# Optimization experiments

Measured on AMD Instinct MI355X. Metric: run time of the kernel, lower is better.

## Reference

```python
import jax, jax.numpy as jnp
import numpy as np

NGRAM = 2
NUM_HEADS = 16
NUM_BUCKETS = 32
EMBED_DIM = 1024
REAL_T = 512
BSZ = 4


def setup_inputs() -> dict:
    key = jax.random.key(0)
    ks = jax.random.split(key, 10)
    tgt_len = (1 + NGRAM) * REAL_T
    E, H, NB = EMBED_DIM, NUM_HEADS, NUM_BUCKETS
    w = 0.02
    return {
        "query": jax.random.normal(ks[0], (tgt_len, BSZ, E), jnp.float32),
        "self_attn_mask": jnp.zeros((REAL_T, REAL_T), jnp.float32),
        "ngram_mask_matrix": jnp.zeros((NGRAM, REAL_T, 2 * REAL_T), jnp.float32),
        "i_buckets_main_stream": jax.random.randint(ks[1], (BSZ, REAL_T, REAL_T), 0, NB, jnp.int32),
        "i_bucket_relative_stream": jax.random.randint(ks[2], (BSZ, REAL_T, 2 * REAL_T), 0, NB, jnp.int32),
        "in_proj_weight": jax.random.normal(ks[3], (3 * E, E), jnp.float32) * w,
        "in_proj_bias": jnp.zeros((3 * E,), jnp.float32),
        "out_proj_weight": jax.random.normal(ks[4], (E, E), jnp.float32) * w,
        "out_proj_bias": jnp.zeros((E,), jnp.float32),
        "relative_weight": jax.random.normal(ks[5], (NB * H, E), jnp.float32) * w,
        "relative_bias": jnp.zeros((NB * H,), jnp.float32),
    }


def _forward(query, self_attn_mask, ngram_mask_matrix,
             ib_main, ib_rel,
             in_proj_weight, in_proj_bias, out_proj_weight, out_proj_bias,
             relative_weight, relative_bias):
    tgt_len, bsz, E = query.shape
    H, n = NUM_HEADS, NGRAM
    hd = E // H
    nb = relative_weight.shape[0] // H
    T = tgt_len // (1 + n)
    scaling = hd ** -0.5

    # fused qkv projection
    qkv = query @ in_proj_weight.T + in_proj_bias  # [tgt, B, 3E]
    q, k, v = jnp.split(qkv, 3, axis=-1)
    q = q * scaling

    def to_bh(x):  # [tgt, B, E] -> [B*H, tgt, hd]
        return x.reshape(tgt_len, bsz * H, hd).transpose(1, 0, 2)
    q, k, v = to_bh(q), to_bh(k), to_bh(v)

    h_main = query[:T]                                  # [T, B, E]
    h_pred = query[T:].reshape(n, T, bsz, E)            # [n, T, B, E]
    q_main, k_main, v_main = q[:, :T], k[:, :T], v[:, :T]            # [BH, T, hd]
    def pred(x):  # [BH, n*T, hd] -> [n, BH, T, hd]
        return x[:, T:].reshape(bsz * H, n, T, hd).transpose(1, 0, 2, 3)
    q_pred, k_pred, v_pred = pred(q), pred(k), pred(v)

    # ---- main stream ----
    aw_main = jnp.einsum('bth,bsh->bts', q_main, k_main)  # [BH, T, T]
    # relative bias: per-token bucket values gathered by bucket index
    vals_main = h_main.transpose(1, 0, 2) @ relative_weight.T + relative_bias  # [B, T, nb*H]
    vals_main = vals_main.reshape(bsz, T, nb, H).transpose(0, 3, 1, 2)         # [B, H, T, nb]
    ib = jnp.broadcast_to(ib_main[:, None].astype(jnp.int32), (bsz, H, T, T))
    rel_main = jnp.take_along_axis(vals_main, ib, axis=-1).reshape(bsz * H, T, T)
    aw_main = aw_main + rel_main + self_attn_mask[None]
    p_main = jax.nn.softmax(aw_main, axis=-1)
    attn_main = jnp.einsum('bts,bsh->bth', p_main, v_main)  # [BH, T, hd]
    attn_main = attn_main.transpose(1, 0, 2).reshape(T, bsz, E)

    # ---- ngram predict streams ----
    k_ng = jnp.concatenate([jnp.broadcast_to(k_main[None], (n,) + k_main.shape), k_pred], axis=2)  # [n, BH, 2T, hd]
    v_ng = jnp.concatenate([jnp.broadcast_to(v_main[None], (n,) + v_main.shape), v_pred], axis=2)
    aw_ng = jnp.einsum('nbtc,nbsc->nbts', q_pred, k_ng)  # [n, BH, T, 2T]

    vals_ng = h_pred.transpose(0, 2, 1, 3) @ relative_weight.T + relative_bias  # [n, B, T, nb*H]
    vals_ng = vals_ng.reshape(n, bsz, T, nb, H).transpose(0, 1, 4, 2, 3)        # [n, B, H, T, nb]
    ibr = jnp.broadcast_to(ib_rel[None, :, None].astype(jnp.int32), (n, bsz, H, T, 2 * T))
    rel_ng = jnp.take_along_axis(vals_ng, ibr, axis=-1).reshape(n, bsz * H, T, 2 * T)
    aw_ng = aw_ng + rel_ng + ngram_mask_matrix[:, None]
    p_ng = jax.nn.softmax(aw_ng, axis=-1)
    attn_ng = jnp.einsum('nbts,nbsc->nbtc', p_ng, v_ng)  # [n, BH, T, hd]
    attn_ng = attn_ng.transpose(0, 2, 1, 3).reshape(n * T, bsz, E)

    attn = jnp.concatenate([attn_main, attn_ng], axis=0)  # [tgt, B, E]
    return attn @ out_proj_weight.T + out_proj_bias


def reference(query, self_attn_mask, ngram_mask_matrix,
              i_buckets_main_stream, i_bucket_relative_stream,
              in_proj_weight, in_proj_bias, out_proj_weight, out_proj_bias,
              relative_weight, relative_bias):
    return _forward(query, self_attn_mask, ngram_mask_matrix,
                    i_buckets_main_stream, i_bucket_relative_stream,
                    in_proj_weight, in_proj_bias, out_proj_weight, out_proj_bias,
                    relative_weight, relative_bias)
```

## Files before the change

### kernel.cpp

```cpp
#include <hip/hip_runtime.h>

#define TSEQ 512
#define BSZN 4
#define NH 16
#define NBN 32
#define EMB 1024
#define HD 64
#define TGT 1536
#define MROWS 6144
#define LOG2E 1.44269504088896f

typedef unsigned short ushort_t;
typedef __bf16 bf8 __attribute__((ext_vector_type(8)));
typedef __bf16 bf2_t __attribute__((ext_vector_type(2)));
typedef ushort_t u16x8v __attribute__((ext_vector_type(8)));
typedef unsigned int u32x2 __attribute__((ext_vector_type(2)));
typedef float f32x4 __attribute__((ext_vector_type(4)));

__device__ __forceinline__ unsigned short f2bf(float f) {
  return __builtin_bit_cast(unsigned short, (__bf16)f);
}

__device__ __forceinline__ float bf2f(unsigned short u) {
  return __builtin_bit_cast(float, (unsigned int)u << 16);
}

__device__ __forceinline__ unsigned int packbf(float a, float b) {
  bf2_t t;
  t[0] = (__bf16)a;
  t[1] = (__bf16)b;
  return __builtin_bit_cast(unsigned int, t);
}

__device__ __forceinline__ void gload16(const void* g, void* l) {
  __builtin_amdgcn_global_load_lds(
      (const __attribute__((address_space(1))) void*)g,
      (__attribute__((address_space(3))) void*)l, 16, 0, 0);
}

__device__ __forceinline__ f32x4 mfma_bf16(bf8 a, bf8 b, f32x4 c) {
  return __builtin_amdgcn_mfma_f32_16x16x32_bf16(a, b, c, 0, 0, 0);
}

__device__ __forceinline__ float lanebcast(float v, int srclane) {
  return __builtin_bit_cast(float,
      __builtin_amdgcn_ds_bpermute(srclane * 4, __builtin_bit_cast(int, v)));
}

__global__ void prep_all_kernel(const float* __restrict__ q, const float* __restrict__ win,
                                const float* __restrict__ wout, const float* __restrict__ wrel,
                                const int* __restrict__ ibm, const int* __restrict__ ibr,
                                const float* __restrict__ mm, const float* __restrict__ mng,
                                ushort_t* __restrict__ qo, ushort_t* __restrict__ wino,
                                ushort_t* __restrict__ wouto, ushort_t* __restrict__ wrelo,
                                unsigned int* __restrict__ cm, unsigned int* __restrict__ cng) {
  const int i = blockIdx.x * blockDim.x + threadIdx.x;
  const int n0 = 1572864, n1 = 786432, n2 = 262144, n3 = 131072;
  const int ncvt = n0 + n1 + n2 + n3;
  const int nm = 262144, nr = 1048576;
  if (i < ncvt) {
    const float* src;
    ushort_t* dst;
    int off;
    if (i < n0) { src = q; dst = qo; off = i; }
    else if (i < n0 + n1) { src = win; dst = wino; off = i - n0; }
    else if (i < n0 + n1 + n2) { src = wout; dst = wouto; off = i - n0 - n1; }
    else { src = wrel; dst = wrelo; off = i - n0 - n1 - n2; }
    const float4 v = reinterpret_cast<const float4*>(src)[off];
    ushort4 o;
    o.x = f2bf(v.x); o.y = f2bf(v.y); o.z = f2bf(v.z); o.w = f2bf(v.w);
    reinterpret_cast<ushort4*>(dst)[off] = o;
  } else if (i < ncvt + nm) {
    const int f = (i - ncvt) * 4;
    const int4 ib = *reinterpret_cast<const int4*>(ibm + f);
    const float4 mk = *reinterpret_cast<const float4*>(mm + (f & 262143));
    uint4 o;
    o.x = ((unsigned int)f2bf(mk.x * LOG2E) << 16) | ((unsigned int)ib.x & 31u);
    o.y = ((unsigned int)f2bf(mk.y * LOG2E) << 16) | ((unsigned int)ib.y & 31u);
    o.z = ((unsigned int)f2bf(mk.z * LOG2E) << 16) | ((unsigned int)ib.z & 31u);
    o.w = ((unsigned int)f2bf(mk.w * LOG2E) << 16) | ((unsigned int)ib.w & 31u);
    *reinterpret_cast<uint4*>(cm + f) = o;
  } else if (i < ncvt + nm + nr) {
    const int f = (i - ncvt - nm) * 4;
    const int ib_off = ((f >> 20) << 19) + (f & 524287);
    const int mk_off = f & 1048575;
    const int4 ib = *reinterpret_cast<const int4*>(ibr + ib_off);
    const float4 mk = *reinterpret_cast<const float4*>(mng + mk_off);
    uint4 o;
    o.x = ((unsigned int)f2bf(mk.x * LOG2E) << 16) | ((unsigned int)ib.x & 31u);
    o.y = ((unsigned int)f2bf(mk.y * LOG2E) << 16) | ((unsigned int)ib.y & 31u);
    o.z = ((unsigned int)f2bf(mk.z * LOG2E) << 16) | ((unsigned int)ib.z & 31u);
    o.w = ((unsigned int)f2bf(mk.w * LOG2E) << 16) | ((unsigned int)ib.w & 31u);
    *reinterpret_cast<uint4*>(cng + f) = o;
  }
}

template <int MODE>
__global__ __launch_bounds__(256) void gemm_bt(
    const ushort_t* __restrict__ A, const ushort_t* __restrict__ B,
    const float* __restrict__ bias, float* __restrict__ Cf,
    ushort_t* __restrict__ Qo, ushort_t* __restrict__ Ko, ushort_t* __restrict__ Vto,
    int M, int N, int K) {
  __shared__ ushort_t lds[16384];
  ushort_t* lA = lds;
  ushort_t* lB = lds + 8192;

  const int tid = threadIdx.x;
  const int lane = tid & 63;
  const int wid = tid >> 6;
  const int l15 = lane & 15, l4 = lane >> 4;
  const int bm = blockIdx.y, bn = blockIdx.x;
  const int wm = (wid >> 1) * 64, wn = (wid & 1) * 64;

  f32x4 acc[4][4] = {};

  const int r8 = tid >> 3;
  const int c8 = ((tid & 7) ^ (r8 & 7)) * 8;
  const ushort_t* Ag = A + (size_t)(bm * 128 + r8) * K + c8;
  const ushort_t* Bg = B + (size_t)(bn * 128 + r8) * K + c8;
  ushort_t* lAp = lA + tid * 8;
  ushort_t* lBp = lB + tid * 8;

  for (int kt = 0; kt < K; kt += 64) {
    __syncthreads();
#pragma unroll
    for (int i = 0; i < 4; ++i) {
      gload16(Ag + (size_t)i * 32 * K + kt, lAp + i * 2048);
      gload16(Bg + (size_t)i * 32 * K + kt, lBp + i * 2048);
    }
    __syncthreads();
#pragma unroll
    for (int k0 = 0; k0 < 2; ++k0) {
      bf8 af[4], bv[4];
#pragma unroll
      for (int mi = 0; mi < 4; ++mi) {
        const int row = wm + mi * 16 + l15;
        const int slot = (k0 * 4 + l4) ^ (row & 7);
        af[mi] = *reinterpret_cast<const bf8*>(lA + row * 64 + slot * 8);
      }
#pragma unroll
      for (int ni = 0; ni < 4; ++ni) {
        const int row = wn + ni * 16 + l15;
        const int slot = (k0 * 4 + l4) ^ (row & 7);
        bv[ni] = *reinterpret_cast<const bf8*>(lB + row * 64 + slot * 8);
      }
#pragma unroll
      for (int mi = 0; mi < 4; ++mi)
#pragma unroll
        for (int ni = 0; ni < 4; ++ni)
          acc[mi][ni] = mfma_bf16(af[mi], bv[ni], acc[mi][ni]);
    }
  }

  if (MODE == 0 && bn >= 16) {
    __syncthreads();
    char* tb = reinterpret_cast<char*>(lds);
#pragma unroll
    for (int ni = 0; ni < 4; ++ni) {
      const int colloc = wn + ni * 16 + l15;
      const float bc = bias[bn * 128 + colloc];
      const unsigned int swz = (colloc & 7) << 4;
#pragma unroll
      for (int mi = 0; mi < 4; ++mi) {
        const int t_loc = (wm >> 2) + mi * 4 + l4;
        f32x4 v = acc[mi][ni];
#pragma unroll
        for (int r = 0; r < 4; ++r) {
          const int byteoff = colloc * 256 + ((r * 64 + t_loc * 2) ^ swz);
          *reinterpret_cast<ushort_t*>(tb + byteoff) = f2bf(v[r] + bc);
        }
      }
    }
    __syncthreads();
    const int tglob0 = bm * 32;
#pragma unroll
    for (int p = 0; p < 2; ++p) {
      const int pair = wid * 2 + p;
      const int bb = pair >> 1;
      const int hl = pair & 1;
      const int hh = (bn - 16) * 2 + hl;
      const int bh = bb * NH + hh;
      const int tch = lane & 3;
#pragma unroll
      for (int ii = 0; ii < 4; ++ii) {
        const int dloc = ii * 16 + (lane >> 2);
        const int colloc = hl * 64 + dloc;
        const int byteoff = colloc * 256 + ((bb * 64 + tch * 16) ^ ((colloc & 7) << 4));
        const u16x8v val = *reinterpret_cast<const u16x8v*>(tb + byteoff);
        *reinterpret_cast<u16x8v*>(
            Vto + ((size_t)bh * HD + dloc) * TGT + tglob0 + tch * 8) = val;
      }
    }
    return;
  }

#pragma unroll
  for (int ni = 0; ni < 4; ++ni) {
    const int col = bn * 128 + wn + ni * 16 + l15;
    const float bc = bias[col];
#pragma unroll
    for (int mi = 0; mi < 4; ++mi) {
      const int row0 = bm * 128 + wm + mi * 16 + l4 * 4;
      f32x4 v = acc[mi][ni];
#pragma unroll
      for (int r = 0; r < 4; ++r) {
        const int row = row0 + r;
        float val = v[r] + bc;
        if (MODE == 0) {
          const int part = col >> 10;
          const int cc = col & 1023;
          const int h = cc >> 6, d = cc & 63;
          const int t = row >> 2, bb = row & 3;
          const int bh = bb * NH + h;
          if (part == 0) {
            Qo[((size_t)bh * TGT + t) * HD + d] = f2bf(val * (0.125f * LOG2E));
          } else {
            Ko[((size_t)bh * TGT + t) * HD + d] = f2bf(val);
          }
        } else if (MODE == 3) {
          const int hh = col & 15, nb = col >> 4;
          const int qg = row >> 2, bb2 = row & 3;
          Qo[(((size_t)(bb2 * NH + hh)) * TGT + qg) * NBN + nb] = f2bf(val * LOG2E);
        } else {
          Cf[(size_t)row * N + col] = val;
        }
      }
    }
  }
}

__global__ __launch_bounds__(256, 3) void attn_kernel(
    const ushort_t* __restrict__ Q, const ushort_t* __restrict__ Kb,
    const ushort_t* __restrict__ Vt, const ushort_t* __restrict__ VMh,
    const unsigned int* __restrict__ comb_main, const unsigned int* __restrict__ comb_ng,
    ushort_t* __restrict__ AT) {
  __shared__ unsigned char kbuf[2][8192];
  __shared__ unsigned char vbuf[2][8192];
  __shared__ ushort_t vmt[4][1024];
  __shared__ unsigned int pbl[4][512];

  const int tid = threadIdx.x;
  const int lane = tid & 63, wid = tid >> 6;
  const int l15 = lane & 15, l4 = lane >> 4;

  const int n = blockIdx.x;
  const int xcd = n & 7;
  const int b = xcd >> 1;
  const int idx = (xcd & 1) * 96 + (n >> 3);
  const int h = idx / 12;
  const int rem = idx - h * 12;
  const int z = rem >> 2;
  const int blk = rem & 3;
  const int g = (z == 0) ? 0 : z - 1;
  const int bh = b * NH + h;
  const int t0 = blk * 128 + wid * 32;
  const int qrow0 = (z == 0) ? t0 : TSEQ + g * TSEQ + t0;
  const int nsb = (z == 0) ? 8 : 16;

  gload16(VMh + ((size_t)bh * TGT + qrow0 + (lane >> 2)) * NBN + (lane & 3) * 8,
          (ushort_t*)vmt[wid] + lane * 8);
  gload16(VMh + ((size_t)bh * TGT + qrow0 + 16 + (lane >> 2)) * NBN + (lane & 3) * 8,
          (ushort_t*)vmt[wid] + 512 + lane * 8);

  bf8 qf[2][2];
#pragma unroll
  for (int th = 0; th < 2; ++th)
#pragma unroll
    for (int hf = 0; hf < 2; ++hf)
      qf[th][hf] = *reinterpret_cast<const bf8*>(
          &Q[((size_t)bh * TGT + qrow0 + th * 16 + l15) * HD + hf * 32 + l4 * 8]);

  const unsigned int* cb[2];
  {
    const unsigned int* cbase = (z == 0)
        ? comb_main + (size_t)b * TSEQ * TSEQ
        : comb_ng + (size_t)(b * 2 + g) * TSEQ * (2 * TSEQ);
    const int sstr = (z == 0) ? TSEQ : 2 * TSEQ;
    cb[0] = cbase + (size_t)(t0 + l15) * sstr;
    cb[1] = cbase + (size_t)(t0 + 16 + l15) * sstr;
  }

  float m_run[2] = {-1e30f, -1e30f};
  float l_run[2] = {0.f, 0.f};
  f32x4 oacc[2][4] = {};

  const int r8 = lane >> 3;
  const int swzs = ((lane & 7) ^ r8) << 4;
  const int swzr = (l15 & 7) << 4;
  const int swz2 = (l15 & 7) << 2;

  auto stage = [&](int sb, int bf) {
    const int srow0 = (sb < 8) ? sb * 64 : TSEQ + g * TSEQ + (sb - 8) * 64;
    const ushort_t* ks = Kb + ((size_t)bh * TGT + srow0 + wid * 16 + r8) * HD + (swzs >> 1);
    gload16(ks, &kbuf[bf][wid * 2048 + lane * 16]);
    gload16(ks + 8 * HD, &kbuf[bf][wid * 2048 + 1024 + lane * 16]);
    const ushort_t* vs = Vt + ((size_t)bh * HD + wid * 16 + r8) * TGT + srow0 + (swzs >> 1);
    gload16(vs, &vbuf[bf][wid * 2048 + lane * 16]);
    gload16(vs + 8 * TGT, &vbuf[bf][wid * 2048 + 1024 + lane * 16]);
  };

  stage(0, 0);
  asm volatile("s_waitcnt vmcnt(0)" ::: "memory");
  __builtin_amdgcn_s_barrier();

  int cur = 0;
  for (int sb = 0; sb < nsb; ++sb) {
    const int scol = sb * 64;
    if (sb + 1 < nsb) stage(sb + 1, cur ^ 1);

    const unsigned char* kb = kbuf[cur];
    const unsigned char* vbb = vbuf[cur];

    bf8 kf[4][2];
#pragma unroll
    for (int j = 0; j < 4; ++j) {
      const int row = j * 16 + l15;
      kf[j][0] = *reinterpret_cast<const bf8*>(kb + row * 128 + ((l4 * 16) ^ swzr));
      kf[j][1] = *reinterpret_cast<const bf8*>(kb + row * 128 + ((64 + l4 * 16) ^ swzr));
    }

#pragma unroll
    for (int th = 0; th < 2; ++th) {
      const unsigned int* cwp = cb[th] + scol + l4 * 4;
      const uint4 c0 = *reinterpret_cast<const uint4*>(cwp);
      const uint4 c1 = *reinterpret_cast<const uint4*>(cwp + 16);
      const uint4 c2 = *reinterpret_cast<const uint4*>(cwp + 32);
      const uint4 c3 = *reinterpret_cast<const uint4*>(cwp + 48);
      const unsigned int cwa[4][4] = {{c0.x, c0.y, c0.z, c0.w},
                                      {c1.x, c1.y, c1.z, c1.w},
                                      {c2.x, c2.y, c2.z, c2.w},
                                      {c3.x, c3.y, c3.z, c3.w}};
      f32x4 st[4];
#pragma unroll
      for (int j = 0; j < 4; ++j) {
        f32x4 s4 = {};
        s4 = mfma_bf16(kf[j][0], qf[th][0], s4);
        s4 = mfma_bf16(kf[j][1], qf[th][1], s4);
        st[j] = s4;
      }
      const ushort_t* vrow = vmt[wid] + (th * 16 + l15) * 32;
      float vals[4][4];
      float mx = -1e30f;
#pragma unroll
      for (int j = 0; j < 4; ++j) {
#pragma unroll
        for (int r = 0; r < 4; ++r) {
          const unsigned int w = cwa[j][r];
          const float v = st[j][r] + __builtin_bit_cast(float, w & 0xffff0000u) +
                          bf2f(vrow[w & 31u]);
          vals[j][r] = v;
          mx = fmaxf(mx, v);
        }
      }
      mx = fmaxf(mx, __shfl_xor(mx, 16));
      mx = fmaxf(mx, __shfl_xor(mx, 32));

      const float oldm = m_run[th];
      if (!__all(mx - oldm <= 8.f)) {
        const float newm = fmaxf(oldm, mx);
        const float fct = (oldm <= -1e30f) ? 0.f : exp2f(oldm - newm);
        f32x4 rs;
        rs[0] = lanebcast(fct, l4 * 4 + 0);
        rs[1] = lanebcast(fct, l4 * 4 + 1);
        rs[2] = lanebcast(fct, l4 * 4 + 2);
        rs[3] = lanebcast(fct, l4 * 4 + 3);
#pragma unroll
        for (int dt = 0; dt < 4; ++dt) oacc[th][dt] *= rs;
        l_run[th] *= fct;
        m_run[th] = newm;
      }
      const float mref = m_run[th];

      float lsum = 0.f;
#pragma unroll
      for (int j = 0; j < 4; ++j) {
        const float p0 = exp2f(vals[j][0] - mref);
        const float p1 = exp2f(vals[j][1] - mref);
        const float p2 = exp2f(vals[j][2] - mref);
        const float p3 = exp2f(vals[j][3] - mref);
        lsum += (p0 + p1) + (p2 + p3);
        u32x2 pw;
        pw[0] = packbf(p0, p1);
        pw[1] = packbf(p2, p3);
        *reinterpret_cast<u32x2*>(&pbl[wid][l15 * 32 + ((j * 8 + l4 * 2) ^ swz2)]) = pw;
      }
      lsum += __shfl_xor(lsum, 16);
      lsum += __shfl_xor(lsum, 32);
      l_run[th] += lsum;

      const unsigned char* pbase = reinterpret_cast<const unsigned char*>(&pbl[wid][0]);
#pragma unroll
      for (int k32 = 0; k32 < 2; ++k32) {
        const bf8 pa = *reinterpret_cast<const bf8*>(
            pbase + l15 * 128 + ((k32 * 64 + l4 * 16) ^ swzr));
#pragma unroll
        for (int dt = 0; dt < 4; ++dt) {
          const bf8 vb = *reinterpret_cast<const bf8*>(
              vbb + (dt * 16 + l15) * 128 + ((k32 * 64 + l4 * 16) ^ swzr));
          oacc[th][dt] = mfma_bf16(pa, vb, oacc[th][dt]);
        }
      }
    }

    asm volatile("s_waitcnt vmcnt(0)" ::: "memory");
    __builtin_amdgcn_s_barrier();
    cur ^= 1;
  }

#pragma unroll
  for (int th = 0; th < 2; ++th) {
    const float linv = 1.f / l_run[th];
    f32x4 bs;
    bs[0] = lanebcast(linv, l4 * 4 + 0);
    bs[1] = lanebcast(linv, l4 * 4 + 1);
    bs[2] = lanebcast(linv, l4 * 4 + 2);
    bs[3] = lanebcast(linv, l4 * 4 + 3);
#pragma unroll
    for (int dt = 0; dt < 4; ++dt) {
#pragma unroll
      for (int r = 0; r < 4; ++r) {
        const int tout = qrow0 + th * 16 + l4 * 4 + r;
        AT[((size_t)tout * BSZN + b) * EMB + h * HD + dt * 16 + l15] =
            f2bf(oacc[th][dt][r] * bs[r]);
      }
    }
  }
}

extern "C" void kernel_launch(void* const* d_in, const int* in_sizes, int n_in,
                              void* d_out, int out_size, void* d_ws, size_t ws_size,
                              hipStream_t stream) {
  const float* query     = (const float*)d_in[0];
  const float* mask_main = (const float*)d_in[1];
  const float* mask_ng   = (const float*)d_in[2];
  const int*   ib_main   = (const int*)d_in[3];
  const int*   ib_rel    = (const int*)d_in[4];
  const float* w_in      = (const float*)d_in[5];
  const float* b_in      = (const float*)d_in[6];
  const float* w_out     = (const float*)d_in[7];
  const float* b_out     = (const float*)d_in[8];
  const float* w_rel     = (const float*)d_in[9];
  const float* b_rel     = (const float*)d_in[10];
  float* out = (float*)d_out;

  ushort_t* qbf    = (ushort_t*)d_ws;
  ushort_t* winbf  = qbf + 6291456;
  ushort_t* woutbf = winbf + 3145728;
  ushort_t* relwbf = woutbf + 1048576;
  ushort_t* Qb     = relwbf + 524288;
  ushort_t* Kbuf   = Qb + 6291456;
  ushort_t* Vtb    = Kbuf + 6291456;
  ushort_t* VMh    = Vtb + 6291456;
  unsigned int* comb_main = (unsigned int*)(VMh + 3145728);
  unsigned int* comb_ng   = comb_main + 1048576;
  ushort_t* AT     = qbf;

  {
    const int total = 2752512 + 262144 + 1048576;
    prep_all_kernel<<<(total + 255) / 256, 256, 0, stream>>>(
        query, w_in, w_out, w_rel, ib_main, ib_rel, mask_main, mask_ng,
        qbf, winbf, woutbf, relwbf, comb_main, comb_ng);
  }

  gemm_bt<0><<<dim3(24, 48), 256, 0, stream>>>(qbf, winbf, b_in, nullptr,
                                               Qb, Kbuf, Vtb, MROWS, 3072, 1024);
  gemm_bt<3><<<dim3(4, 48), 256, 0, stream>>>(qbf, relwbf, b_rel, nullptr,
                                              VMh, nullptr, nullptr, MROWS, 512, 1024);
  attn_kernel<<<768, 256, 0, stream>>>(Qb, Kbuf, Vtb, VMh, comb_main, comb_ng, AT);
  gemm_bt<2><<<dim3(8, 48), 256, 0, stream>>>(AT, woutbf, b_out, out,
                                              nullptr, nullptr, nullptr, MROWS, 1024, 1024);
}
```

Measured before the change: 212.9 us.

## Transpose P via ds_bpermute and store relative-bias table as padded fp32

The P matrix is no longer round-tripped through a per-wave LDS buffer. Packed bf16 probabilities are redistributed directly between lanes with ds_bpermute plus a select, so they land in the A-operand layout for the PV MFMA. The per-row relative-bucket table is also converted to fp32 once at load, with a padded stride of 36, which removes a bf16-to-fp32 conversion from the inner loop and may reduce bank conflicts. In exchange there are 8 bpermutes per k32 step, each still an LDS-path operation, where there used to be one store and one read, and the vm table doubles in LDS size.

```diff
diff --git a/kernel.cpp b/kernel.cpp
--- a/kernel.cpp
+++ b/kernel.cpp
@@ -14,7 +14,7 @@
 typedef __bf16 bf8 __attribute__((ext_vector_type(8)));
 typedef __bf16 bf2_t __attribute__((ext_vector_type(2)));
 typedef ushort_t u16x8v __attribute__((ext_vector_type(8)));
-typedef unsigned int u32x2 __attribute__((ext_vector_type(2)));
+typedef unsigned int u32x4v __attribute__((ext_vector_type(4)));
 typedef float f32x4 __attribute__((ext_vector_type(4)));
 
 __device__ __forceinline__ unsigned short f2bf(float f) {
@@ -236,8 +236,7 @@
     ushort_t* __restrict__ AT) {
   __shared__ unsigned char kbuf[2][8192];
   __shared__ unsigned char vbuf[2][8192];
-  __shared__ ushort_t vmt[4][1024];
-  __shared__ unsigned int pbl[4][512];
+  __shared__ float vmtf[4][1152];
 
   const int tid = threadIdx.x;
   const int lane = tid & 63, wid = tid >> 6;
@@ -257,10 +256,23 @@
   const int qrow0 = (z == 0) ? t0 : TSEQ + g * TSEQ + t0;
   const int nsb = (z == 0) ? 8 : 16;
 
-  gload16(VMh + ((size_t)bh * TGT + qrow0 + (lane >> 2)) * NBN + (lane & 3) * 8,
-          (ushort_t*)vmt[wid] + lane * 8);
-  gload16(VMh + ((size_t)bh * TGT + qrow0 + 16 + (lane >> 2)) * NBN + (lane & 3) * 8,
-          (ushort_t*)vmt[wid] + 512 + lane * 8);
+  {
+    const ushort_t* src = VMh + ((size_t)bh * TGT + qrow0) * NBN;
+    float* dstf = vmtf[wid];
+#pragma unroll
+    for (int half = 0; half < 2; ++half) {
+      const u16x8v v = *reinterpret_cast<const u16x8v*>(src + half * 512 + lane * 8);
+      const int r = half * 16 + (lane >> 2);
+      const int c0 = (lane & 3) * 8;
+      f32x4 lo, hi;
+#pragma unroll
+      for (int i = 0; i < 4; ++i) lo[i] = bf2f(v[i]);
+#pragma unroll
+      for (int i = 0; i < 4; ++i) hi[i] = bf2f(v[4 + i]);
+      *reinterpret_cast<f32x4*>(dstf + r * 36 + c0) = lo;
+      *reinterpret_cast<f32x4*>(dstf + r * 36 + c0 + 4) = hi;
+    }
+  }
 
   bf8 qf[2][2];
 #pragma unroll
@@ -287,7 +299,9 @@
   const int r8 = lane >> 3;
   const int swzs = ((lane & 7) ^ r8) << 4;
   const int swzr = (l15 & 7) << 4;
-  const int swz2 = (l15 & 7) << 2;
+  const int a0 = l15 * 4 + (l4 & 1) * 128;
+  const int a1 = a0 + 64;
+  const bool hi2 = (l4 & 2) != 0;
 
   auto stage = [&](int sb, int bf) {
     const int srow0 = (sb < 8) ? sb * 64 : TSEQ + g * TSEQ + (sb - 8) * 64;
@@ -338,7 +352,7 @@
         s4 = mfma_bf16(kf[j][1], qf[th][1], s4);
         st[j] = s4;
       }
-      const ushort_t* vrow = vmt[wid] + (th * 16 + l15) * 32;
+      const float* vrow = vmtf[wid] + (th * 16 + l15) * 36;
       float vals[4][4];
       float mx = -1e30f;
 #pragma unroll
@@ -347,7 +361,7 @@
         for (int r = 0; r < 4; ++r) {
           const unsigned int w = cwa[j][r];
           const float v = st[j][r] + __builtin_bit_cast(float, w & 0xffff0000u) +
-                          bf2f(vrow[w & 31u]);
+                          vrow[w & 31u];
           vals[j][r] = v;
           mx = fmaxf(mx, v);
         }
@@ -371,6 +385,7 @@
       }
       const float mref = m_run[th];
 
+      unsigned int pk[4][2];
       float lsum = 0.f;
 #pragma unroll
       for (int j = 0; j < 4; ++j) {
@@ -379,20 +394,31 @@
         const float p2 = exp2f(vals[j][2] - mref);
         const float p3 = exp2f(vals[j][3] - mref);
         lsum += (p0 + p1) + (p2 + p3);
-        u32x2 pw;
-        pw[0] = packbf(p0, p1);
-        pw[1] = packbf(p2, p3);
-        *reinterpret_cast<u32x2*>(&pbl[wid][l15 * 32 + ((j * 8 + l4 * 2) ^ swz2)]) = pw;
+        pk[j][0] = packbf(p0, p1);
+        pk[j][1] = packbf(p2, p3);
       }
       lsum += __shfl_xor(lsum, 16);
       lsum += __shfl_xor(lsum, 32);
       l_run[th] += lsum;
 
-      const unsigned char* pbase = reinterpret_cast<const unsigned char*>(&pbl[wid][0]);
 #pragma unroll
       for (int k32 = 0; k32 < 2; ++k32) {
-        const bf8 pa = *reinterpret_cast<const bf8*>(
-            pbase + l15 * 128 + ((k32 * 64 + l4 * 16) ^ swzr));
+        const int e0 = (int)pk[2 * k32][0], e1 = (int)pk[2 * k32][1];
+        const int o0 = (int)pk[2 * k32 + 1][0], o1 = (int)pk[2 * k32 + 1][1];
+        const unsigned int p0e = (unsigned int)__builtin_amdgcn_ds_bpermute(a0, e0);
+        const unsigned int p0o = (unsigned int)__builtin_amdgcn_ds_bpermute(a0, o0);
+        const unsigned int p1e = (unsigned int)__builtin_amdgcn_ds_bpermute(a0, e1);
+        const unsigned int p1o = (unsigned int)__builtin_amdgcn_ds_bpermute(a0, o1);
+        const unsigned int p2e = (unsigned int)__builtin_amdgcn_ds_bpermute(a1, e0);
+        const unsigned int p2o = (unsigned int)__builtin_amdgcn_ds_bpermute(a1, o0);
+        const unsigned int p3e = (unsigned int)__builtin_amdgcn_ds_bpermute(a1, e1);
+        const unsigned int p3o = (unsigned int)__builtin_amdgcn_ds_bpermute(a1, o1);
+        u32x4v pad;
+        pad[0] = hi2 ? p0o : p0e;
+        pad[1] = hi2 ? p1o : p1e;
+        pad[2] = hi2 ? p2o : p2e;
+        pad[3] = hi2 ? p3o : p3e;
+        const bf8 pa = __builtin_bit_cast(bf8, pad);
 #pragma unroll
         for (int dt = 0; dt < 4; ++dt) {
           const bf8 vb = *reinterpret_cast<const bf8*>(
```

Result: no change. 214.8 us (+0.9%).
